# Performance work log

Measured on AMD Instinct MI355X. Metric: run time of the kernel, lower is better.

## Reference

```python
import jax, jax.numpy as jnp
import numpy as np

N_NODES = 100000
N_EDGES = 1600000
F_IN = 64
HIDDEN = 64
N_CLASSES = 2


def setup_inputs() -> dict:
    key = jax.random.key(0)
    k1, k2, k3, k4, k5, k6 = jax.random.split(key, 6)
    x = jax.random.normal(k1, (N_NODES, F_IN), dtype=jnp.float32)
    edge_index = jax.random.randint(k2, (2, N_EDGES), 0, N_NODES, dtype=jnp.int64)
    # Glorot-ish init for GCNConv linear weights, zero bias (PyG default)
    W1 = jax.random.normal(k3, (F_IN, HIDDEN), dtype=jnp.float32) * (1.0 / np.sqrt(F_IN))
    b1 = jnp.zeros((HIDDEN,), dtype=jnp.float32)
    W2 = jax.random.normal(k4, (HIDDEN, N_CLASSES), dtype=jnp.float32) * (1.0 / np.sqrt(HIDDEN))
    b2 = jnp.zeros((N_CLASSES,), dtype=jnp.float32)
    return {"x": x, "edge_index": edge_index, "W1": W1, "b1": b1, "W2": W2, "b2": b2}


def _gcn_norm(edge_index, num_nodes):
    # Add self-loops, then symmetric normalization D^-1/2 (A+I) D^-1/2
    loops = jnp.arange(num_nodes, dtype=edge_index.dtype)
    row = jnp.concatenate([edge_index[0], loops])  # [E+N] targets
    col = jnp.concatenate([edge_index[1], loops])  # [E+N] sources
    deg = jax.ops.segment_sum(jnp.ones(row.shape[0], jnp.float32), row, num_segments=num_nodes)
    dinv = jnp.where(deg > 0, jax.lax.rsqrt(deg), 0.0)
    norm = dinv[row] * dinv[col]  # [E+N]
    return row, col, norm


def _gcn_conv(x, W, b, row, col, norm, num_nodes):
    h = x @ W                                   # [N, out]
    msg = h[col] * norm[:, None]                # gather + scale, [E+N, out]
    agg = jax.ops.segment_sum(msg, row, num_segments=num_nodes)  # scatter-add
    return agg + b


def reference(x, edge_index, W1, b1, W2, b2):
    n = x.shape[0]
    row, col, norm = _gcn_norm(edge_index, n)
    h = jax.nn.relu(_gcn_conv(x, W1, b1, row, col, norm, n))
    # dropout p=0.5 is identity in eval mode
    logits = _gcn_conv(h, W2, b2, row, col, norm, n)
    return jax.nn.softmax(logits, axis=1)
```

## Files before the change

kernel.cpp:

```cpp
#include <hip/hip_runtime.h>
#include <hip/hip_fp16.h>


typedef _Float16 f16x8 __attribute__((ext_vector_type(8)));
typedef float f32x4 __attribute__((ext_vector_type(4)));

#define CAPSH 13
#define CAP (1 << CAPSH)

__global__ __launch_bounds__(256) void k_bin(const int* __restrict__ row,
                                             const int* __restrict__ col,
                                             int* __restrict__ relcur,
                                             unsigned* __restrict__ pairbuf,
                                             __half* __restrict__ hp,
                                             int E, int nb, int N) {
    __shared__ unsigned items[4096];
    __shared__ unsigned short bktid[4096];
    __shared__ int cnt[392];
    __shared__ int start0[392];
    __shared__ int cursor[392];
    __shared__ int gbase[392];

    int tid = threadIdx.x;
    int base = blockIdx.x * 4096;
    int m = E - base; if (m > 4096) m = 4096;

    for (int t = tid; t < nb; t += 256) cnt[t] = 0;
    __syncthreads();
    for (int i = tid; i < m; i += 256) atomicAdd(&cnt[row[base + i] >> 8], 1);
    __syncthreads();
    if (tid < 64) {
        int lane = tid, running = 0;
        for (int ch = 0; ch < 7; ++ch) {
            int idx = ch * 64 + lane;
            int v = (idx < nb) ? cnt[idx] : 0;
            int s = v;
#pragma unroll
            for (int off = 1; off < 64; off <<= 1) {
                int t = __shfl_up(s, off, 64);
                if (lane >= off) s += t;
            }
            if (idx < nb) { start0[idx] = running + s - v; cursor[idx] = running + s - v; }
            running += __shfl(s, 63, 64);
        }
    }
    __syncthreads();
    for (int i = tid; i < m; i += 256) {
        int r = row[base + i];
        int c = col[base + i];
        int b = r >> 8;
        int pos = atomicAdd(&cursor[b], 1);
        items[pos] = ((unsigned)(r & 255) << 24) | (unsigned)c;
        bktid[pos] = (unsigned short)b;
    }
    __syncthreads();
    for (int t = tid; t < nb; t += 256) {
        int cv = cnt[t];
        if (cv > 0) gbase[t] = (t << CAPSH) + atomicAdd(&relcur[t], cv);
    }
    __syncthreads();
    for (int i = tid; i < m; i += 256) {
        int b = bktid[i];
        pairbuf[gbase[b] + (i - start0[b])] = items[i];
    }
    if (blockIdx.x == 0 && tid < 32) ((int*)(hp + (size_t)N * 64))[tid] = 0;
}

__global__ __launch_bounds__(256, 4) void k_sortgemm(const unsigned* __restrict__ pairbuf,
                                                     const int* __restrict__ relcur,
                                                     const float* __restrict__ x,
                                                     const float* __restrict__ W1,
                                                     int* __restrict__ scol,
                                                     int* __restrict__ offsets,
                                                     int* __restrict__ deg,
                                                     float* __restrict__ dinv,
                                                     __half* __restrict__ hp,
                                                     int N, int nb) {
    __shared__ int cnt[256];
    __shared__ int tmp[256];
    __shared__ int cur[256];
    __shared__ float sdinv[256];
    int b = blockIdx.x;
    int tid = threadIdx.x;
    int lane = tid & 63, q = lane >> 4, mm = lane & 15;
    f16x8 bf[4][2];
#pragma unroll
    for (int nt = 0; nt < 4; ++nt)
#pragma unroll
        for (int kk = 0; kk < 2; ++kk)
#pragma unroll
            for (int j = 0; j < 8; ++j)
                bf[nt][kk][j] = (_Float16)W1[(kk * 32 + q * 8 + j) * 64 + nt * 16 + mm];

    int lo = b << CAPSH;
    int hi = lo + relcur[b];
    cnt[tid] = 0;
    __syncthreads();
    for (int i = lo + tid; i < hi; i += 256)
        atomicAdd(&cnt[pairbuf[i] >> 24], 1);
    __syncthreads();
    int cv = cnt[tid];
    tmp[tid] = cv;
    __syncthreads();
    for (int d = 1; d < 256; d <<= 1) {
        int t = (tid >= d) ? tmp[tid - d] : 0;
        __syncthreads();
        if (tid >= d) tmp[tid] += t;
        __syncthreads();
    }
    int excl = tmp[tid] - cv;
    int n = (b << 8) + tid;
    float dv = rsqrtf((float)(cv + 1));
    if (n < N) { offsets[n] = lo + excl; deg[n] = cv; dinv[n] = dv; }
    sdinv[tid] = dv;
    cur[tid] = lo + excl;
    if (b == 0 && tid == 0) {
        offsets[N] = 0; deg[N] = 0;
        scol[nb << CAPSH] = N;
    }
    __syncthreads();
    for (int i = lo + tid; i < hi; i += 256) {
        unsigned it = pairbuf[i];
        int pos = atomicAdd(&cur[it >> 24], 1);
        scol[pos] = (int)(it & 0xFFFFFFu);
    }
    __syncthreads();
    int n0 = b << 8;
    int nn = N - n0; if (nn > 256) nn = 256;
    for (int t = (tid >> 6); t < (nn >> 4); t += 4) {
        const float* xrow = x + (size_t)(n0 + t * 16 + mm) * 64;
        float4 u0 = *(const float4*)(xrow + q * 8);
        float4 u1 = *(const float4*)(xrow + q * 8 + 4);
        float4 u2 = *(const float4*)(xrow + 32 + q * 8);
        float4 u3 = *(const float4*)(xrow + 32 + q * 8 + 4);
        f16x8 a0, a1;
        a0[0] = (_Float16)u0.x; a0[1] = (_Float16)u0.y; a0[2] = (_Float16)u0.z; a0[3] = (_Float16)u0.w;
        a0[4] = (_Float16)u1.x; a0[5] = (_Float16)u1.y; a0[6] = (_Float16)u1.z; a0[7] = (_Float16)u1.w;
        a1[0] = (_Float16)u2.x; a1[1] = (_Float16)u2.y; a1[2] = (_Float16)u2.z; a1[3] = (_Float16)u2.w;
        a1[4] = (_Float16)u3.x; a1[5] = (_Float16)u3.y; a1[6] = (_Float16)u3.z; a1[7] = (_Float16)u3.w;
        f32x4 ac0 = {0.f, 0.f, 0.f, 0.f}, ac1 = ac0, ac2 = ac0, ac3 = ac0;
        ac0 = __builtin_amdgcn_mfma_f32_16x16x32_f16(a0, bf[0][0], ac0, 0, 0, 0);
        ac1 = __builtin_amdgcn_mfma_f32_16x16x32_f16(a0, bf[1][0], ac1, 0, 0, 0);
        ac2 = __builtin_amdgcn_mfma_f32_16x16x32_f16(a0, bf[2][0], ac2, 0, 0, 0);
        ac3 = __builtin_amdgcn_mfma_f32_16x16x32_f16(a0, bf[3][0], ac3, 0, 0, 0);
        ac0 = __builtin_amdgcn_mfma_f32_16x16x32_f16(a1, bf[0][1], ac0, 0, 0, 0);
        ac1 = __builtin_amdgcn_mfma_f32_16x16x32_f16(a1, bf[1][1], ac1, 0, 0, 0);
        ac2 = __builtin_amdgcn_mfma_f32_16x16x32_f16(a1, bf[2][1], ac2, 0, 0, 0);
        ac3 = __builtin_amdgcn_mfma_f32_16x16x32_f16(a1, bf[3][1], ac3, 0, 0, 0);
#pragma unroll
        for (int reg = 0; reg < 4; ++reg) {
            int rl = t * 16 + q * 4 + reg;
            float dvv = sdinv[rl];
            __half* dst = hp + (size_t)(n0 + rl) * 64 + mm;
            dst[0]  = __float2half(dvv * ac0[reg]);
            dst[16] = __float2half(dvv * ac1[reg]);
            dst[32] = __float2half(dvv * ac2[reg]);
            dst[48] = __float2half(dvv * ac3[reg]);
        }
    }
}

__global__ __launch_bounds__(256, 4) void k_agg1(const __half* __restrict__ hp,
                                                 const int* __restrict__ offsets,
                                                 const int* __restrict__ deg,
                                                 const int* __restrict__ scol,
                                                 const float* __restrict__ dinv,
                                                 const float* __restrict__ b1,
                                                 const float* __restrict__ W2,
                                                 float2* __restrict__ h2p,
                                                 int N, int SENT) {
    int lane = threadIdx.x & 63;
    int slot = lane >> 3;
    int chunk = lane & 7;
    int wid = (int)((blockIdx.x * 256 + threadIdx.x) >> 6);
    int n = wid * 8 + slot;
    int nc = (n < N) ? n : N;
    int start = offsets[nc];
    int dg = deg[nc];
    int maxd = dg;
#pragma unroll
    for (int s = 8; s <= 32; s <<= 1) {
        int o = __shfl_xor(maxd, s, 64);
        maxd = (o > maxd) ? o : maxd;
    }
    const float4* hp4 = (const float4*)hp;
    float4 sr = hp4[(size_t)nc * 8 + chunk];
    __half2 acc0 = ((const __half2*)&sr)[0];
    __half2 acc1 = ((const __half2*)&sr)[1];
    __half2 acc2 = ((const __half2*)&sr)[2];
    __half2 acc3 = ((const __half2*)&sr)[3];
    for (int j0 = 0; j0 < maxd; j0 += 8) {
        int c[8];
#pragma unroll
        for (int u = 0; u < 8; ++u)
            c[u] = scol[(j0 + u < dg) ? (start + j0 + u) : SENT];
        float4 r[8];
#pragma unroll
        for (int u = 0; u < 8; ++u) r[u] = hp4[(size_t)c[u] * 8 + chunk];
#pragma unroll
        for (int u = 0; u < 8; ++u) {
            const __half2* hh = (const __half2*)&r[u];
            acc0 = __hadd2(acc0, hh[0]); acc1 = __hadd2(acc1, hh[1]);
            acc2 = __hadd2(acc2, hh[2]); acc3 = __hadd2(acc3, hh[3]);
        }
    }
    float af[8];
    { float2 f;
      f = __half22float2(acc0); af[0] = f.x; af[1] = f.y;
      f = __half22float2(acc1); af[2] = f.x; af[3] = f.y;
      f = __half22float2(acc2); af[4] = f.x; af[5] = f.y;
      f = __half22float2(acc3); af[6] = f.x; af[7] = f.y; }
    float dn = dinv[(n < N) ? n : (N - 1)];
    float4 b1a = ((const float4*)b1)[chunk * 2];
    float4 b1b = ((const float4*)b1)[chunk * 2 + 1];
    float h1[8];
    h1[0] = fmaxf(fmaf(dn, af[0], b1a.x), 0.f);
    h1[1] = fmaxf(fmaf(dn, af[1], b1a.y), 0.f);
    h1[2] = fmaxf(fmaf(dn, af[2], b1a.z), 0.f);
    h1[3] = fmaxf(fmaf(dn, af[3], b1a.w), 0.f);
    h1[4] = fmaxf(fmaf(dn, af[4], b1b.x), 0.f);
    h1[5] = fmaxf(fmaf(dn, af[5], b1b.y), 0.f);
    h1[6] = fmaxf(fmaf(dn, af[6], b1b.z), 0.f);
    h1[7] = fmaxf(fmaf(dn, af[7], b1b.w), 0.f);
    float p0 = 0.f, p1 = 0.f;
#pragma unroll
    for (int k = 0; k < 4; ++k) {
        float4 w = ((const float4*)W2)[chunk * 4 + k];
        p0 = fmaf(h1[2 * k], w.x, p0); p1 = fmaf(h1[2 * k], w.y, p1);
        p0 = fmaf(h1[2 * k + 1], w.z, p0); p1 = fmaf(h1[2 * k + 1], w.w, p1);
    }
#pragma unroll
    for (int s = 1; s <= 4; s <<= 1) {
        p0 += __shfl_xor(p0, s, 64);
        p1 += __shfl_xor(p1, s, 64);
    }
    if (chunk == 0 && n < N) h2p[n] = make_float2(dn * p0, dn * p1);
}

__global__ __launch_bounds__(256) void k_agg2(const float2* __restrict__ h2p,
                                              const int* __restrict__ offsets,
                                              const int* __restrict__ deg,
                                              const int* __restrict__ scol,
                                              const float* __restrict__ dinv,
                                              const float* __restrict__ b2,
                                              float2* __restrict__ out, int N) {
    int gtid = blockIdx.x * 256 + threadIdx.x;
    int n = gtid >> 4;
    int sub = threadIdx.x & 15;
    if (n >= N) return;
    int start = offsets[n], end = start + deg[n];
    float ax = 0.f, ay = 0.f;
    if (sub == 0) { float2 s = h2p[n]; ax = s.x; ay = s.y; }
    for (int j = start + sub; j < end; j += 16) {
        float2 v = h2p[scol[j]];
        ax += v.x; ay += v.y;
    }
#pragma unroll
    for (int s = 1; s <= 8; s <<= 1) {
        ax += __shfl_xor(ax, s, 64);
        ay += __shfl_xor(ay, s, 64);
    }
    if (sub == 0) {
        float dn = dinv[n];
        float l0 = fmaf(dn, ax, b2[0]), l1 = fmaf(dn, ay, b2[1]);
        float m = fmaxf(l0, l1);
        float e0 = __expf(l0 - m), e1 = __expf(l1 - m);
        float inv = 1.0f / (e0 + e1);
        out[n] = make_float2(e0 * inv, e1 * inv);
    }
}

extern "C" void kernel_launch(void* const* d_in, const int* in_sizes, int n_in,
                              void* d_out, int out_size, void* d_ws, size_t ws_size,
                              hipStream_t stream) {
    const float* x  = (const float*)d_in[0];
    const int*   ei = (const int*)d_in[1];
    const float* W1 = (const float*)d_in[2];
    const float* b1 = (const float*)d_in[3];
    const float* W2 = (const float*)d_in[4];
    const float* b2 = (const float*)d_in[5];
    float2* out = (float2*)d_out;

    const int N = in_sizes[0] / 64;
    const int E = in_sizes[1] / 2;
    const int nb = (N + 255) >> 8;
    const int SENT = nb << CAPSH;
    const int* row = ei;
    const int* col = ei + E;

    char* p = (char*)d_ws;
    auto alloc = [&](size_t bytes) -> void* {
        void* r = (void*)p;
        p += (bytes + 255) & ~(size_t)255;
        return r;
    };
    int*   relcur  = (int*)alloc((size_t)nb * 4);
    int*   offsets = (int*)alloc((size_t)(N + 1) * 4);
    int*   deg     = (int*)alloc((size_t)(N + 1) * 4);
    float* dinv    = (float*)alloc((size_t)N * 4);
    unsigned* pairbuf = (unsigned*)alloc((size_t)nb * CAP * 4);
    int*   scol    = (int*)alloc(((size_t)nb * CAP + 1) * 4);
    __half* hp     = (__half*)alloc((size_t)(N + 1) * 64 * 2);
    float2* h2p    = (float2*)alloc((size_t)N * 8);

    const int nTile = (E + 4095) / 4096;

    hipMemsetAsync(relcur, 0, (size_t)nb * 4, stream);
    k_bin<<<nTile, 256, 0, stream>>>(row, col, relcur, pairbuf, hp, E, nb, N);
    k_sortgemm<<<nb, 256, 0, stream>>>(pairbuf, relcur, x, W1, scol, offsets, deg, dinv, hp, N, nb);
    const int nwaves = (N + 7) / 8;
    k_agg1<<<(nwaves + 3) / 4, 256, 0, stream>>>(hp, offsets, deg, scol, dinv, b1, W2, h2p, N, SENT);
    k_agg2<<<(N * 16 + 255) / 256, 256, 0, stream>>>(h2p, offsets, deg, scol, dinv, b2, out, N);
}
```

Measured before the change: 165.7 us.

## Degree-sort nodes per bucket for balanced aggregation; halve binning tile size

In the sort/GEMM kernel, each 256-node bucket now ranks its nodes by in-degree and writes a permutation array. Both aggregation kernels walk nodes in that order, so the 8 nodes sharing a wave have similar degrees and less lane time is lost waiting on the longest neighbour list. The binning kernel tile also shrinks from 4096 to 2048 edges, giving more blocks. The cost is an O(256) rank loop per thread, an extra indirection load in both aggregation kernels, and scattered writes to h2p and the output.

Result: slower. 190.6 us (+15.0%).

```diff
diff --git a/kernel.cpp b/kernel.cpp
--- a/kernel.cpp
+++ b/kernel.cpp
@@ -14,16 +14,16 @@
                                              unsigned* __restrict__ pairbuf,
                                              __half* __restrict__ hp,
                                              int E, int nb, int N) {
-    __shared__ unsigned items[4096];
-    __shared__ unsigned short bktid[4096];
+    __shared__ unsigned items[2048];
+    __shared__ unsigned short bktid[2048];
     __shared__ int cnt[392];
     __shared__ int start0[392];
     __shared__ int cursor[392];
     __shared__ int gbase[392];
 
     int tid = threadIdx.x;
-    int base = blockIdx.x * 4096;
-    int m = E - base; if (m > 4096) m = 4096;
+    int base = blockIdx.x * 2048;
+    int m = E - base; if (m > 2048) m = 2048;
 
     for (int t = tid; t < nb; t += 256) cnt[t] = 0;
     __syncthreads();
@@ -74,6 +74,7 @@
                                                      int* __restrict__ offsets,
                                                      int* __restrict__ deg,
                                                      float* __restrict__ dinv,
+                                                     int* __restrict__ pperm,
                                                      __half* __restrict__ hp,
                                                      int N, int nb) {
     __shared__ int cnt[256];
@@ -94,6 +95,8 @@
 
     int lo = b << CAPSH;
     int hi = lo + relcur[b];
+    int n0 = b << 8;
+    int nn = N - n0; if (nn > 256) nn = 256;
     cnt[tid] = 0;
     __syncthreads();
     for (int i = lo + tid; i < hi; i += 256)
@@ -109,7 +112,7 @@
         __syncthreads();
     }
     int excl = tmp[tid] - cv;
-    int n = (b << 8) + tid;
+    int n = n0 + tid;
     float dv = rsqrtf((float)(cv + 1));
     if (n < N) { offsets[n] = lo + excl; deg[n] = cv; dinv[n] = dv; }
     sdinv[tid] = dv;
@@ -125,8 +128,18 @@
         scol[pos] = (int)(it & 0xFFFFFFu);
     }
     __syncthreads();
-    int n0 = b << 8;
-    int nn = N - n0; if (nn > 256) nn = 256;
+    int myd = (tid < nn) ? cv : 0x7FFFFFFF;
+    tmp[tid] = myd;
+    __syncthreads();
+    int rank = 0;
+    for (int j = 0; j < 256; ++j) {
+        int dj = tmp[j];
+        rank += (dj < myd) || (dj == myd && j < tid);
+    }
+    cnt[rank] = tid;
+    __syncthreads();
+    int node = n0 + cnt[tid];
+    pperm[n0 + tid] = (node < N) ? node : N;
     for (int t = (tid >> 6); t < (nn >> 4); t += 4) {
         const float* xrow = x + (size_t)(n0 + t * 16 + mm) * 64;
         float4 u0 = *(const float4*)(xrow + q * 8);
@@ -167,16 +180,17 @@
                                                  const float* __restrict__ dinv,
                                                  const float* __restrict__ b1,
                                                  const float* __restrict__ W2,
+                                                 const int* __restrict__ pperm,
                                                  float2* __restrict__ h2p,
-                                                 int N, int SENT) {
+                                                 int N, int SENT, int NP) {
     int lane = threadIdx.x & 63;
     int slot = lane >> 3;
     int chunk = lane & 7;
     int wid = (int)((blockIdx.x * 256 + threadIdx.x) >> 6);
-    int n = wid * 8 + slot;
-    int nc = (n < N) ? n : N;
-    int start = offsets[nc];
-    int dg = deg[nc];
+    int idx = wid * 8 + slot;
+    int node = (idx < NP) ? pperm[idx] : N;
+    int start = offsets[node];
+    int dg = deg[node];
     int maxd = dg;
 #pragma unroll
     for (int s = 8; s <= 32; s <<= 1) {
@@ -184,7 +198,7 @@
         maxd = (o > maxd) ? o : maxd;
     }
     const float4* hp4 = (const float4*)hp;
-    float4 sr = hp4[(size_t)nc * 8 + chunk];
+    float4 sr = hp4[(size_t)node * 8 + chunk];
     __half2 acc0 = ((const __half2*)&sr)[0];
     __half2 acc1 = ((const __half2*)&sr)[1];
     __half2 acc2 = ((const __half2*)&sr)[2];
@@ -210,7 +224,7 @@
       f = __half22float2(acc1); af[2] = f.x; af[3] = f.y;
       f = __half22float2(acc2); af[4] = f.x; af[5] = f.y;
       f = __half22float2(acc3); af[6] = f.x; af[7] = f.y; }
-    float dn = dinv[(n < N) ? n : (N - 1)];
+    float dn = dinv[(node < N) ? node : 0];
     float4 b1a = ((const float4*)b1)[chunk * 2];
     float4 b1b = ((const float4*)b1)[chunk * 2 + 1];
     float h1[8];
@@ -234,7 +248,7 @@
         p0 += __shfl_xor(p0, s, 64);
         p1 += __shfl_xor(p1, s, 64);
     }
-    if (chunk == 0 && n < N) h2p[n] = make_float2(dn * p0, dn * p1);
+    if (chunk == 0 && node < N) h2p[node] = make_float2(dn * p0, dn * p1);
 }
 
 __global__ __launch_bounds__(256) void k_agg2(const float2* __restrict__ h2p,
@@ -243,10 +257,13 @@
                                               const int* __restrict__ scol,
                                               const float* __restrict__ dinv,
                                               const float* __restrict__ b2,
-                                              float2* __restrict__ out, int N) {
+                                              const int* __restrict__ pperm,
+                                              float2* __restrict__ out, int N, int NP) {
     int gtid = blockIdx.x * 256 + threadIdx.x;
-    int n = gtid >> 4;
+    int t = gtid >> 4;
     int sub = threadIdx.x & 15;
+    if (t >= NP) return;
+    int n = pperm[t];
     if (n >= N) return;
     int start = offsets[n], end = start + deg[n];
     float ax = 0.f, ay = 0.f;
@@ -284,6 +301,7 @@
     const int N = in_sizes[0] / 64;
     const int E = in_sizes[1] / 2;
     const int nb = (N + 255) >> 8;
+    const int NP = nb << 8;
     const int SENT = nb << CAPSH;
     const int* row = ei;
     const int* col = ei + E;
@@ -298,17 +316,18 @@
     int*   offsets = (int*)alloc((size_t)(N + 1) * 4);
     int*   deg     = (int*)alloc((size_t)(N + 1) * 4);
     float* dinv    = (float*)alloc((size_t)N * 4);
+    int*   pperm   = (int*)alloc((size_t)NP * 4);
     unsigned* pairbuf = (unsigned*)alloc((size_t)nb * CAP * 4);
     int*   scol    = (int*)alloc(((size_t)nb * CAP + 1) * 4);
     __half* hp     = (__half*)alloc((size_t)(N + 1) * 64 * 2);
     float2* h2p    = (float2*)alloc((size_t)N * 8);
 
-    const int nTile = (E + 4095) / 4096;
+    const int nTile = (E + 2047) / 2048;
 
     hipMemsetAsync(relcur, 0, (size_t)nb * 4, stream);
     k_bin<<<nTile, 256, 0, stream>>>(row, col, relcur, pairbuf, hp, E, nb, N);
-    k_sortgemm<<<nb, 256, 0, stream>>>(pairbuf, relcur, x, W1, scol, offsets, deg, dinv, hp, N, nb);
-    const int nwaves = (N + 7) / 8;
-    k_agg1<<<(nwaves + 3) / 4, 256, 0, stream>>>(hp, offsets, deg, scol, dinv, b1, W2, h2p, N, SENT);
-    k_agg2<<<(N * 16 + 255) / 256, 256, 0, stream>>>(h2p, offsets, deg, scol, dinv, b2, out, N);
-}
+    k_sortgemm<<<nb, 256, 0, stream>>>(pairbuf, relcur, x, W1, scol, offsets, deg, dinv, pperm, hp, N, nb);
+    const int nwaves = NP / 8;
+    k_agg1<<<(nwaves + 3) / 4, 256, 0, stream>>>(hp, offsets, deg, scol, dinv, b1, W2, pperm, h2p, N, SENT, NP);
+    k_agg2<<<(NP * 16 + 255) / 256, 256, 0, stream>>>(h2p, offsets, deg, scol, dinv, b2, pperm, out, N, NP);
+}
```
